# Optimization experiments

Measured on AMD Instinct MI355X. Metric: run time of the kernel, lower is better.

Reference implementation:

```python
import jax, jax.numpy as jnp
import numpy as np

B, T, H, M = 16, 1024, 512, 80
NHEADS, HDIM = 8, H // 8


def _p(key, shape, scale=0.05):
    return scale * jax.random.normal(key, shape, dtype=jnp.float32)


def setup_inputs() -> dict:
    key = jax.random.key(0)
    ks = jax.random.split(key, 20)
    return {
        "encoder_memory": jax.random.normal(ks[0], (B, T, H), dtype=jnp.float32),
        "target_mel": jax.random.normal(ks[1], (B, T, M), dtype=jnp.float32),
        # prenet Linear(mel_dim -> hidden_dim)
        "w_prenet": _p(ks[2], (H, M)), "b_prenet": _p(ks[3], (H,)),
        # MultiheadAttention packed in-proj (3H, H) and out-proj (H, H)
        "in_proj_w": _p(ks[4], (3 * H, H)), "in_proj_b": _p(ks[5], (3 * H,)),
        "out_proj_w": _p(ks[6], (H, H)), "out_proj_b": _p(ks[7], (H,)),
        # 2-layer LSTM (torch gate order i,f,g,o); h0=c0=0 each step so W_hh acts on zeros
        "w_ih0": _p(ks[8], (4 * H, 2 * H)), "w_hh0": _p(ks[9], (4 * H, H)),
        "b_ih0": _p(ks[10], (4 * H,)), "b_hh0": _p(ks[11], (4 * H,)),
        "w_ih1": _p(ks[12], (4 * H, H)), "w_hh1": _p(ks[13], (4 * H, H)),
        "b_ih1": _p(ks[14], (4 * H,)), "b_hh1": _p(ks[15], (4 * H,)),
        # mel projection Linear(hidden_dim -> mel_dim)
        "w_mel": _p(ks[16], (M, H)), "b_mel": _p(ks[17], (M,)),
    }


def _lstm_cell_zero_state(x, w_ih, w_hh, b_ih, b_hh):
    # single step from zero (h, c): the W_hh @ h0 term is exactly zero
    gates = x @ w_ih.T + (b_ih + b_hh)  # (B,T,4H)
    i, f, g, o = jnp.split(gates, 4, axis=-1)
    c = jax.nn.sigmoid(i) * jnp.tanh(g)  # f * c_prev == 0
    return jax.nn.sigmoid(o) * jnp.tanh(c)


def reference(encoder_memory, target_mel, w_prenet, b_prenet,
              in_proj_w, in_proj_b, out_proj_w, out_proj_b,
              w_ih0, w_hh0, b_ih0, b_hh0, w_ih1, w_hh1, b_ih1, b_hh1,
              w_mel, b_mel):
    # teacher forcing: prev_mel at step t is zeros (t=0) else target_mel[:, t-1]
    prev = jnp.concatenate(
        [jnp.zeros((B, 1, M), dtype=target_mel.dtype), target_mel[:, :-1]], axis=1)
    pre = jax.nn.relu(prev @ w_prenet.T + b_prenet)  # (B,T,H); dropout is identity (eval)

    # cross-attention: each step's length-1 query attends over all encoder frames,
    # which vectorizes to standard (no-mask) MHA with queries = pre
    wq, wk, wv = jnp.split(in_proj_w, 3, axis=0)
    bq, bk, bv = jnp.split(in_proj_b, 3, axis=0)
    q = (pre @ wq.T + bq).reshape(B, T, NHEADS, HDIM)
    k = (encoder_memory @ wk.T + bk).reshape(B, T, NHEADS, HDIM)
    v = (encoder_memory @ wv.T + bv).reshape(B, T, NHEADS, HDIM)
    scale = 1.0 / jnp.sqrt(jnp.float32(HDIM))
    scores = jnp.einsum('bqhd,bkhd->bhqk', q * scale, k)  # (B,8,T,T)
    attn = jax.nn.softmax(scores, axis=-1)
    ctx = jnp.einsum('bhqk,bkhd->bqhd', attn, v).reshape(B, T, H)
    attn_out = ctx @ out_proj_w.T + out_proj_b  # (B,T,H)

    dec_in = jnp.concatenate([pre, attn_out], axis=-1)  # (B,T,2H)
    h1 = _lstm_cell_zero_state(dec_in, w_ih0, w_hh0, b_ih0, b_hh0)
    h2 = _lstm_cell_zero_state(h1, w_ih1, w_hh1, b_ih1, b_hh1)
    return h2 @ w_mel.T + b_mel  # (B,T,M)
```

## Files before the change

### kernel.cpp

```cpp
#include <hip/hip_runtime.h>


typedef _Float16 f16;
typedef _Float16 f16x8 __attribute__((ext_vector_type(8)));
typedef _Float16 f16x4 __attribute__((ext_vector_type(4)));
typedef float f32x4 __attribute__((ext_vector_type(4)));

constexpr int B_ = 16, T_ = 1024, H_ = 512, M_ = 80;
constexpr int NH_ = 8, D_ = 64;
constexpr int N_ = B_ * T_;

#define MFMA16(a, b, c) __builtin_amdgcn_mfma_f32_16x16x32_f16(a, b, c, 0, 0, 0)

__device__ __forceinline__ void gload_lds16(const f16* g, f16* l) {
  __builtin_amdgcn_global_load_lds(
      (const __attribute__((address_space(1))) void*)g,
      (__attribute__((address_space(3))) void*)l, 16, 0, 0);
}

template <int EPI, bool CONCATA, bool NCHK>
__global__ __launch_bounds__(256) void mgemm(
    const f16* __restrict__ A, const f16* __restrict__ A2,
    const f16* __restrict__ Wt, const float* __restrict__ bias,
    const float* __restrict__ bias2, float scale, void* __restrict__ outp,
    int K, int N) {
  __shared__ f16 As[128 * 64];
  __shared__ f16 Bs[128 * 64];
  const int tid = threadIdx.x;
  const int lane = tid & 63, wid = tid >> 6;
  const int lq = lane & 15, lg = lane >> 4;
  const int wm = wid >> 1, wn = wid & 1;
  const int r0 = blockIdx.x * 128, c0 = blockIdx.y * 128;

  f32x4 acc[4][4] = {};

  for (int k0 = 0; k0 < K; k0 += 64) {
#pragma unroll
    for (int it = 0; it < 4; ++it) {
      const int off = it * 4096 + wid * 1024 + lane * 16;
      const int row = off >> 7;
      const int cb = (off >> 4) & 7;
      const int kc = k0 + ((cb ^ (row & 7)) << 3);
      const f16* src;
      if (CONCATA) {
        src = (kc < 512) ? (A + (size_t)(r0 + row) * 512 + kc)
                         : (A2 + (size_t)(r0 + row) * 512 + (kc - 512));
      } else {
        src = A + (size_t)(r0 + row) * K + kc;
      }
      gload_lds16(src, (f16*)((char*)As + off));
    }
#pragma unroll
    for (int it = 0; it < 4; ++it) {
      const int off = it * 4096 + wid * 1024 + lane * 16;
      const int row = off >> 7;
      const int cb = (off >> 4) & 7;
      int crow = c0 + row;
      if (NCHK) crow = crow < N ? crow : N - 1;
      gload_lds16(Wt + (size_t)crow * K + k0 + ((cb ^ (row & 7)) << 3),
                  (f16*)((char*)Bs + off));
    }
    __syncthreads();
#pragma unroll
    for (int kk = 0; kk < 2; ++kk) {
      f16x8 af[4], bf[4];
#pragma unroll
      for (int m = 0; m < 4; ++m) {
        const int row = wm * 64 + m * 16 + lq;
        af[m] = *(const f16x8*)((const char*)As + row * 128 +
                                (((kk * 4 + lg) ^ (row & 7)) << 4));
      }
#pragma unroll
      for (int n = 0; n < 4; ++n) {
        const int row = wn * 64 + n * 16 + lq;
        bf[n] = *(const f16x8*)((const char*)Bs + row * 128 +
                                (((kk * 4 + lg) ^ (row & 7)) << 4));
      }
#pragma unroll
      for (int m = 0; m < 4; ++m)
#pragma unroll
        for (int n = 0; n < 4; ++n) acc[m][n] = MFMA16(af[m], bf[n], acc[m][n]);
    }
    __syncthreads();
  }

#pragma unroll
  for (int m = 0; m < 4; ++m) {
    const int rbase = r0 + wm * 64 + m * 16 + lg * 4;
#pragma unroll
    for (int n = 0; n < 4; ++n) {
      const int col = c0 + wn * 64 + n * 16 + lq;
      if (NCHK && col >= N) continue;
      const float bsum = bias[col] + (bias2 ? bias2[col] : 0.f);
      const f32x4 a = acc[m][n];
      if (EPI == 3) {
        const int b = rbase >> 10, t = rbase & (T_ - 1);
        const int head = col >> 6, d = col & 63;
        f16x4 pk;
#pragma unroll
        for (int r = 0; r < 4; ++r) pk[r] = (f16)((a[r] + bsum) * scale);
        *(f16x4*)((f16*)outp + ((size_t)((b * NH_ + head) * D_ + d)) * T_ + t) =
            pk;
      } else {
#pragma unroll
        for (int r = 0; r < 4; ++r) {
          const int row = rbase + r;
          float v = (a[r] + bsum) * scale;
          if (EPI == 1) v = fmaxf(v, 0.f);
          if (EPI == 4)
            ((float*)outp)[(size_t)row * N + col] = v;
          else
            ((f16*)outp)[(size_t)row * N + col] = (f16)v;
        }
      }
    }
  }
}

template <bool CONCATA>
__global__ __launch_bounds__(512) void lstm_fused(
    const f16* __restrict__ A, const f16* __restrict__ A2,
    const f16* __restrict__ Wih, const float* __restrict__ bih,
    const float* __restrict__ bhh, f16* __restrict__ Hout_) {
  constexpr int K = CONCATA ? 1024 : 512;
  __shared__ f16 As[128 * 64];
  __shared__ f16 Bs[3][128 * 64];
  const int tid = threadIdx.x;
  const int lane = tid & 63, wid = tid >> 6;
  const int lq = lane & 15, lg = lane >> 4;
  const int wm = wid >> 1, wn = wid & 1;
  const int r0 = blockIdx.x * 128, c0 = blockIdx.y * 128;

  f32x4 acc[3][2][4] = {};

  for (int k0 = 0; k0 < K; k0 += 64) {
#pragma unroll
    for (int it = 0; it < 2; ++it) {
      const int off = it * 8192 + tid * 16;
      const int row = off >> 7;
      const int cb = (off >> 4) & 7;
      const int kc = k0 + ((cb ^ (row & 7)) << 3);
      const f16* src;
      if (CONCATA) {
        src = (kc < 512) ? (A + (size_t)(r0 + row) * 512 + kc)
                         : (A2 + (size_t)(r0 + row) * 512 + (kc - 512));
      } else {
        src = A + (size_t)(r0 + row) * K + kc;
      }
      gload_lds16(src, (f16*)((char*)As + off));
    }
#pragma unroll
    for (int g = 0; g < 3; ++g) {
      const int gbase = (g == 0) ? 0 : 512 * (g + 1);
#pragma unroll
      for (int it = 0; it < 2; ++it) {
        const int off = it * 8192 + tid * 16;
        const int row = off >> 7;
        const int cb = (off >> 4) & 7;
        gload_lds16(
            Wih + (size_t)(gbase + c0 + row) * K + k0 + ((cb ^ (row & 7)) << 3),
            (f16*)((char*)&Bs[g][0] + off));
      }
    }
    __syncthreads();
#pragma unroll
    for (int kk = 0; kk < 2; ++kk) {
      f16x8 af[2];
#pragma unroll
      for (int m = 0; m < 2; ++m) {
        const int row = wm * 32 + m * 16 + lq;
        af[m] = *(const f16x8*)((const char*)As + row * 128 +
                                (((kk * 4 + lg) ^ (row & 7)) << 4));
      }
#pragma unroll
      for (int g = 0; g < 3; ++g)
#pragma unroll
        for (int n = 0; n < 4; ++n) {
          const int row = wn * 64 + n * 16 + lq;
          const f16x8 bf = *(const f16x8*)((const char*)&Bs[g][0] + row * 128 +
                                           (((kk * 4 + lg) ^ (row & 7)) << 4));
#pragma unroll
          for (int m = 0; m < 2; ++m)
            acc[g][m][n] = MFMA16(af[m], bf, acc[g][m][n]);
        }
    }
    __syncthreads();
  }

#pragma unroll
  for (int n = 0; n < 4; ++n) {
    const int c = c0 + wn * 64 + n * 16 + lq;
    const float bi = bih[c] + bhh[c];
    const float bg = bih[1024 + c] + bhh[1024 + c];
    const float bo = bih[1536 + c] + bhh[1536 + c];
#pragma unroll
    for (int m = 0; m < 2; ++m) {
      const int rbase = r0 + wm * 32 + m * 16 + lg * 4;
#pragma unroll
      for (int r = 0; r < 4; ++r) {
        const float gi = acc[0][m][n][r] + bi;
        const float gg = acc[1][m][n][r] + bg;
        const float go = acc[2][m][n][r] + bo;
        const float si = 1.f / (1.f + __expf(-gi));
        const float so = 1.f / (1.f + __expf(-go));
        const float tg = 2.f / (1.f + __expf(-2.f * gg)) - 1.f;
        const float cc = si * tg;
        const float tc = 2.f / (1.f + __expf(-2.f * cc)) - 1.f;
        Hout_[(size_t)(rbase + r) * 512 + c] = (f16)(so * tc);
      }
    }
  }
}

__global__ __launch_bounds__(256) void attn_mfma3(
    const f16* __restrict__ q, const f16* __restrict__ k,
    const f16* __restrict__ vT, f16* __restrict__ ctx) {
  __shared__ f16 Ks[2][64 * 64];
  __shared__ f16 Vs[2][64 * 64];
  __shared__ f16 Ps[4][16 * 64];
  const int qt = blockIdx.x, head = blockIdx.y, b = blockIdx.z;
  const int tid = threadIdx.x, lane = tid & 63, wid = tid >> 6;
  const int lq = lane & 15, lg = lane >> 4;
  const int bh = b * NH_ + head;

  const f16* kbase = k + ((size_t)b * T_) * H_ + head * D_;
  const f16* vbase = vT + (size_t)bh * D_ * T_;

  auto stage = [&](int kt, int buf) {
#pragma unroll
    for (int it = 0; it < 2; ++it) {
      const int off = it * 4096 + tid * 16;
      const int row = off >> 7;
      const int sc = ((((off >> 4) & 7) ^ (row & 7)) << 3);
      gload_lds16(kbase + (size_t)(kt * 64 + row) * H_ + sc,
                  (f16*)((char*)&Ks[buf][0] + off));
      gload_lds16(vbase + (size_t)row * T_ + kt * 64 + sc,
                  (f16*)((char*)&Vs[buf][0] + off));
    }
  };

  const int q0 = qt * 128 + wid * 32;
  f16x8 qf[2][2];
#pragma unroll
  for (int s = 0; s < 2; ++s)
#pragma unroll
    for (int kk = 0; kk < 2; ++kk)
      qf[s][kk] = *(const f16x8*)(q + ((size_t)(b * T_) + q0 + s * 16 + lq) * H_ +
                                  head * D_ + kk * 32 + lg * 8);

  float m_run[2] = {-1e30f, -1e30f}, l_run[2] = {0.f, 0.f};
  f32x4 accO[2][4] = {};
  char* pw = (char*)&Ps[wid][0] + lq * 128;
  const int psw = (lq & 3) << 5;

  stage(0, 0);
  __syncthreads();

  for (int kt = 0; kt < T_ / 64; ++kt) {
    const int cur = kt & 1;
    if (kt < T_ / 64 - 1) stage(kt + 1, cur ^ 1);

    f16x8 kf[4][2];
#pragma unroll
    for (int n = 0; n < 4; ++n)
#pragma unroll
      for (int kk = 0; kk < 2; ++kk) {
        const int row = n * 16 + lq;
        kf[n][kk] = *(const f16x8*)((const char*)&Ks[cur][0] + row * 128 +
                                    (((kk * 4 + lg) ^ (row & 7)) << 4));
      }
    f32x4 ssw[2][4] = {};
    __builtin_amdgcn_s_setprio(1);
#pragma unroll
    for (int s = 0; s < 2; ++s)
#pragma unroll
      for (int n = 0; n < 4; ++n)
#pragma unroll
        for (int kk = 0; kk < 2; ++kk)
          ssw[s][n] = MFMA16(kf[n][kk], qf[s][kk], ssw[s][n]);
    __builtin_amdgcn_s_setprio(0);

    f16x8 vf[4][2];
#pragma unroll
    for (int n = 0; n < 4; ++n)
#pragma unroll
      for (int kk = 0; kk < 2; ++kk) {
        const int row = n * 16 + lq;
        vf[n][kk] = *(const f16x8*)((const char*)&Vs[cur][0] + row * 128 +
                                    (((kk * 4 + lg) ^ (row & 7)) << 4));
      }

#pragma unroll
    for (int s = 0; s < 2; ++s) {
      float mloc = -1e30f;
#pragma unroll
      for (int n = 0; n < 4; ++n)
#pragma unroll
        for (int r = 0; r < 4; ++r) mloc = fmaxf(mloc, ssw[s][n][r]);
      mloc = fmaxf(mloc, __shfl_xor(mloc, 16, 64));
      mloc = fmaxf(mloc, __shfl_xor(mloc, 32, 64));

      const bool noresc = __all(mloc - m_run[s] <= 8.f);
      if (!noresc) {
        const float nm = fmaxf(m_run[s], mloc);
        const float corr = __expf(m_run[s] - nm);
        m_run[s] = nm;
        l_run[s] *= corr;
#pragma unroll
        for (int n = 0; n < 4; ++n) {
          accO[s][n][0] *= corr; accO[s][n][1] *= corr;
          accO[s][n][2] *= corr; accO[s][n][3] *= corr;
        }
      }
      float sl = 0.f;
#pragma unroll
      for (int n = 0; n < 4; ++n) {
        f16x4 pk;
#pragma unroll
        for (int r = 0; r < 4; ++r) {
          const float p = __expf(ssw[s][n][r] - m_run[s]);
          sl += p;
          pk[r] = (f16)p;
        }
        *(f16x4*)(pw + ((n * 32 + lg * 8) ^ psw)) = pk;
      }
      sl += __shfl_xor(sl, 16, 64);
      sl += __shfl_xor(sl, 32, 64);
      l_run[s] += sl;

      f16x8 pb[2];
#pragma unroll
      for (int kk = 0; kk < 2; ++kk)
        pb[kk] = *(const f16x8*)(pw + ((((kk * 4 + lg) << 4)) ^ psw));
      __builtin_amdgcn_s_setprio(1);
#pragma unroll
      for (int n = 0; n < 4; ++n)
#pragma unroll
        for (int kk = 0; kk < 2; ++kk)
          accO[s][n] = MFMA16(vf[n][kk], pb[kk], accO[s][n]);
      __builtin_amdgcn_s_setprio(0);
    }
    __syncthreads();
  }

#pragma unroll
  for (int s = 0; s < 2; ++s) {
    const float inv = 1.f / l_run[s];
    const size_t rowoff = ((size_t)(b * T_) + q0 + s * 16 + lq) * H_ + head * D_;
#pragma unroll
    for (int n = 0; n < 4; ++n) {
      f16x4 o;
#pragma unroll
      for (int r = 0; r < 4; ++r) o[r] = (f16)(accO[s][n][r] * inv);
      *(f16x4*)(ctx + rowoff + n * 16 + lg * 4) = o;
    }
  }
}

constexpr int C0 = 2097152;
constexpr int C1 = C0 + 196608;
constexpr int C2 = C1 + 65536;
constexpr int C3 = C2 + 524288;
constexpr int C4 = C3 + 262144;
constexpr int C5 = C4 + 10240;
__global__ void conv_all(const float* __restrict__ enc, const float* __restrict__ inw,
                         const float* __restrict__ outw, const float* __restrict__ wih0,
                         const float* __restrict__ wih1, const float* __restrict__ wmel,
                         f16* denc, f16* dinw, f16* doutw, f16* dwih0,
                         f16* dwih1, f16* dwmel) {
  const int i = blockIdx.x * blockDim.x + threadIdx.x;
  const float* s;
  f16* d;
  int off;
  if (i < C0) { s = enc; d = denc; off = i; }
  else if (i < C1) { s = inw; d = dinw; off = i - C0; }
  else if (i < C2) { s = outw; d = doutw; off = i - C1; }
  else if (i < C3) { s = wih0; d = dwih0; off = i - C2; }
  else if (i < C4) { s = wih1; d = dwih1; off = i - C3; }
  else if (i < C5) { s = wmel; d = dwmel; off = i - C4; }
  else return;
  const float4 v = ((const float4*)s)[off];
  f16x4 o = {(f16)v.x, (f16)v.y, (f16)v.z, (f16)v.w};
  ((f16x4*)d)[off] = o;
}

__global__ void build_pm(const float* __restrict__ tmel, f16* __restrict__ pm) {
  const int i = blockIdx.x * blockDim.x + threadIdx.x;
  const int r = i >> 5, c4 = (i & 31) * 4;
  const int t = r & (T_ - 1);
  f16x4 o = {};
  if (t != 0 && c4 < M_) {
    const float4 v = *(const float4*)(tmel + (size_t)(r - 1) * M_ + c4);
    o = {(f16)v.x, (f16)v.y, (f16)v.z, (f16)v.w};
  }
  *(f16x4*)(pm + (size_t)r * 128 + c4) = o;
}

__global__ void build_wp(const float* __restrict__ w, f16* __restrict__ wp) {
  const int i = blockIdx.x * blockDim.x + threadIdx.x;
  const int r = i >> 5, c4 = (i & 31) * 4;
  f16x4 o = {};
  if (c4 < M_) {
    const float4 v = *(const float4*)(w + (size_t)r * M_ + c4);
    o = {(f16)v.x, (f16)v.y, (f16)v.z, (f16)v.w};
  }
  *(f16x4*)(wp + (size_t)r * 128 + c4) = o;
}

extern "C" void kernel_launch(void* const* d_in, const int* in_sizes, int n_in,
                              void* d_out, int out_size, void* d_ws,
                              size_t ws_size, hipStream_t stream) {
  const float* enc = (const float*)d_in[0];
  const float* tmel = (const float*)d_in[1];
  const float* w_pre = (const float*)d_in[2];
  const float* b_pre = (const float*)d_in[3];
  const float* inw = (const float*)d_in[4];
  const float* inb = (const float*)d_in[5];
  const float* outw = (const float*)d_in[6];
  const float* outb = (const float*)d_in[7];
  const float* wih0 = (const float*)d_in[8];
  const float* bih0 = (const float*)d_in[10];
  const float* bhh0 = (const float*)d_in[11];
  const float* wih1 = (const float*)d_in[12];
  const float* bih1 = (const float*)d_in[14];
  const float* bhh1 = (const float*)d_in[15];
  const float* wmel = (const float*)d_in[16];
  const float* bmel = (const float*)d_in[17];

  f16* wsh = (f16*)d_ws;
  const size_t SEG = (size_t)N_ * H_;
  f16* EncB = wsh;
  f16* h1 = wsh + SEG;
  f16* pre = wsh + 2 * SEG;
  f16* qb = wsh + 3 * SEG;
  f16* kbuf = wsh + 4 * SEG;
  f16* vTb = wsh + 5 * SEG;
  f16* ctx = wsh + 6 * SEG;
  f16* aout = EncB;
  f16* h2 = qb;
  f16* WP = wsh + 7 * SEG;
  f16* WIN = WP + 512 * 128;
  f16* WOUT = WIN + 1536 * 512;
  f16* WIH0 = WOUT + 512 * 512;
  f16* WIH1 = WIH0 + 2048 * 1024;
  f16* WMEL = WIH1 + 2048 * 512;
  f16* PM = WMEL + 80 * 512;

  const dim3 blk(256);
  conv_all<<<(C5 + 255) / 256, blk, 0, stream>>>(enc, inw, outw, wih0, wih1,
                                                 wmel, EncB, WIN, WOUT, WIH0,
                                                 WIH1, WMEL);
  build_pm<<<(N_ * 32) / 256, blk, 0, stream>>>(tmel, PM);
  build_wp<<<(512 * 32) / 256, blk, 0, stream>>>(w_pre, WP);

  const dim3 g512(N_ / 128, 4), g80(N_ / 128, 1);
  mgemm<1, false, false><<<g512, blk, 0, stream>>>(PM, nullptr, WP, b_pre,
                                                   nullptr, 1.f, pre, 128, 512);
  mgemm<0, false, false><<<g512, blk, 0, stream>>>(pre, nullptr, WIN, inb,
                                                   nullptr, 0.125f, qb, 512, 512);
  mgemm<0, false, false><<<g512, blk, 0, stream>>>(
      EncB, nullptr, WIN + 512 * 512, inb + 512, nullptr, 1.f, kbuf, 512, 512);
  mgemm<3, false, false><<<g512, blk, 0, stream>>>(
      EncB, nullptr, WIN + 1024 * 512, inb + 1024, nullptr, 1.f, vTb, 512, 512);
  attn_mfma3<<<dim3(T_ / 128, NH_, B_), blk, 0, stream>>>(qb, kbuf, vTb, ctx);
  mgemm<0, false, false><<<g512, blk, 0, stream>>>(ctx, nullptr, WOUT, outb,
                                                   nullptr, 1.f, aout, 512, 512);
  lstm_fused<true><<<dim3(N_ / 128, 4), dim3(512), 0, stream>>>(
      pre, aout, WIH0, bih0, bhh0, h1);
  lstm_fused<false><<<dim3(N_ / 128, 4), dim3(512), 0, stream>>>(
      h1, nullptr, WIH1, bih1, bhh1, h2);
  mgemm<4, false, true><<<g80, blk, 0, stream>>>(h2, nullptr, WMEL, bmel,
                                                 nullptr, 1.f, (float*)d_out,
                                                 512, 80);
}
```

Measured before the change: 308.5 us.

## Fuse K and V projections into one GEMM and retile LSTM to 256 threads

Replaces the separate K and V projection GEMMs with one kv_fused kernel that loads each encoder tile once and computes both outputs, writing V in transposed layout. The LSTM gate kernel moves from 512 threads with 2x4 MFMA tiles per wave to 256 threads with 4x4 tiles per wave and a two-blocks-per-CU launch bound. The aim is to halve reads of encoder memory and raise MFMA work per LDS fragment load. The larger accumulator arrays (48 and 32 f32x4 per thread) raise register pressure and may reduce occupancy.

```diff
diff --git a/kernel.cpp b/kernel.cpp
--- a/kernel.cpp
+++ b/kernel.cpp
@@ -118,7 +118,7 @@
 }
 
 template <bool CONCATA>
-__global__ __launch_bounds__(512) void lstm_fused(
+__global__ __launch_bounds__(256, 2) void lstm_fused(
     const f16* __restrict__ A, const f16* __restrict__ A2,
     const f16* __restrict__ Wih, const float* __restrict__ bih,
     const float* __restrict__ bhh, f16* __restrict__ Hout_) {
@@ -131,12 +131,12 @@
   const int wm = wid >> 1, wn = wid & 1;
   const int r0 = blockIdx.x * 128, c0 = blockIdx.y * 128;
 
-  f32x4 acc[3][2][4] = {};
+  f32x4 acc[3][4][4] = {};
 
   for (int k0 = 0; k0 < K; k0 += 64) {
 #pragma unroll
-    for (int it = 0; it < 2; ++it) {
-      const int off = it * 8192 + tid * 16;
+    for (int it = 0; it < 4; ++it) {
+      const int off = it * 4096 + tid * 16;
       const int row = off >> 7;
       const int cb = (off >> 4) & 7;
       const int kc = k0 + ((cb ^ (row & 7)) << 3);
@@ -153,8 +153,8 @@
     for (int g = 0; g < 3; ++g) {
       const int gbase = (g == 0) ? 0 : 512 * (g + 1);
 #pragma unroll
-      for (int it = 0; it < 2; ++it) {
-        const int off = it * 8192 + tid * 16;
+      for (int it = 0; it < 4; ++it) {
+        const int off = it * 4096 + tid * 16;
         const int row = off >> 7;
         const int cb = (off >> 4) & 7;
         gload_lds16(
@@ -165,10 +165,10 @@
     __syncthreads();
 #pragma unroll
     for (int kk = 0; kk < 2; ++kk) {
-      f16x8 af[2];
-#pragma unroll
-      for (int m = 0; m < 2; ++m) {
-        const int row = wm * 32 + m * 16 + lq;
+      f16x8 af[4];
+#pragma unroll
+      for (int m = 0; m < 4; ++m) {
+        const int row = wm * 64 + m * 16 + lq;
         af[m] = *(const f16x8*)((const char*)As + row * 128 +
                                 (((kk * 4 + lg) ^ (row & 7)) << 4));
       }
@@ -180,7 +180,7 @@
           const f16x8 bf = *(const f16x8*)((const char*)&Bs[g][0] + row * 128 +
                                            (((kk * 4 + lg) ^ (row & 7)) << 4));
 #pragma unroll
-          for (int m = 0; m < 2; ++m)
+          for (int m = 0; m < 4; ++m)
             acc[g][m][n] = MFMA16(af[m], bf, acc[g][m][n]);
         }
     }
@@ -194,8 +194,8 @@
     const float bg = bih[1024 + c] + bhh[1024 + c];
     const float bo = bih[1536 + c] + bhh[1536 + c];
 #pragma unroll
-    for (int m = 0; m < 2; ++m) {
-      const int rbase = r0 + wm * 32 + m * 16 + lg * 4;
+    for (int m = 0; m < 4; ++m) {
+      const int rbase = r0 + wm * 64 + m * 16 + lg * 4;
 #pragma unroll
       for (int r = 0; r < 4; ++r) {
         const float gi = acc[0][m][n][r] + bi;
@@ -208,6 +208,88 @@
         const float tc = 2.f / (1.f + __expf(-2.f * cc)) - 1.f;
         Hout_[(size_t)(rbase + r) * 512 + c] = (f16)(so * tc);
       }
+    }
+  }
+}
+
+__global__ __launch_bounds__(256, 2) void kv_fused(
+    const f16* __restrict__ A, const f16* __restrict__ Wt,
+    const float* __restrict__ bias, f16* __restrict__ kout,
+    f16* __restrict__ vout) {
+  constexpr int K = 512;
+  __shared__ f16 As[128 * 64];
+  __shared__ f16 Bs[2][128 * 64];
+  const int tid = threadIdx.x;
+  const int lane = tid & 63, wid = tid >> 6;
+  const int lq = lane & 15, lg = lane >> 4;
+  const int wm = wid >> 1, wn = wid & 1;
+  const int r0 = blockIdx.x * 128, c0 = blockIdx.y * 128;
+
+  f32x4 acc[2][4][4] = {};
+
+  for (int k0 = 0; k0 < K; k0 += 64) {
+#pragma unroll
+    for (int it = 0; it < 4; ++it) {
+      const int off = it * 4096 + tid * 16;
+      const int row = off >> 7;
+      const int cb = (off >> 4) & 7;
+      const int kc = k0 + ((cb ^ (row & 7)) << 3);
+      gload_lds16(A + (size_t)(r0 + row) * K + kc, (f16*)((char*)As + off));
+    }
+#pragma unroll
+    for (int g = 0; g < 2; ++g) {
+#pragma unroll
+      for (int it = 0; it < 4; ++it) {
+        const int off = it * 4096 + tid * 16;
+        const int row = off >> 7;
+        const int cb = (off >> 4) & 7;
+        gload_lds16(
+            Wt + (size_t)(g * 512 + c0 + row) * K + k0 + ((cb ^ (row & 7)) << 3),
+            (f16*)((char*)&Bs[g][0] + off));
+      }
+    }
+    __syncthreads();
+#pragma unroll
+    for (int kk = 0; kk < 2; ++kk) {
+      f16x8 af[4];
+#pragma unroll
+      for (int m = 0; m < 4; ++m) {
+        const int row = wm * 64 + m * 16 + lq;
+        af[m] = *(const f16x8*)((const char*)As + row * 128 +
+                                (((kk * 4 + lg) ^ (row & 7)) << 4));
+      }
+#pragma unroll
+      for (int g = 0; g < 2; ++g)
+#pragma unroll
+        for (int n = 0; n < 4; ++n) {
+          const int row = wn * 64 + n * 16 + lq;
+          const f16x8 bf = *(const f16x8*)((const char*)&Bs[g][0] + row * 128 +
+                                           (((kk * 4 + lg) ^ (row & 7)) << 4));
+#pragma unroll
+          for (int m = 0; m < 4; ++m)
+            acc[g][m][n] = MFMA16(af[m], bf, acc[g][m][n]);
+        }
+    }
+    __syncthreads();
+  }
+
+#pragma unroll
+  for (int m = 0; m < 4; ++m) {
+    const int rbase = r0 + wm * 64 + m * 16 + lg * 4;
+    const int b = rbase >> 10, t = rbase & (T_ - 1);
+#pragma unroll
+    for (int n = 0; n < 4; ++n) {
+      const int col = c0 + wn * 64 + n * 16 + lq;
+      const float bk = bias[col];
+#pragma unroll
+      for (int r = 0; r < 4; ++r)
+        kout[(size_t)(rbase + r) * 512 + col] = (f16)(acc[0][m][n][r] + bk);
+      const float bv = bias[512 + col];
+      const int head = col >> 6, d = col & 63;
+      f16x4 pk;
+#pragma unroll
+      for (int r = 0; r < 4; ++r) pk[r] = (f16)(acc[1][m][n][r] + bv);
+      *(f16x4*)(vout + ((size_t)((b * NH_ + head) * D_ + d)) * T_ + t) = pk;
     }
   }
 }
@@ -458,17 +540,13 @@
                                                    nullptr, 1.f, pre, 128, 512);
   mgemm<0, false, false><<<g512, blk, 0, stream>>>(pre, nullptr, WIN, inb,
                                                    nullptr, 0.125f, qb, 512, 512);
-  mgemm<0, false, false><<<g512, blk, 0, stream>>>(
-      EncB, nullptr, WIN + 512 * 512, inb + 512, nullptr, 1.f, kbuf, 512, 512);
-  mgemm<3, false, false><<<g512, blk, 0, stream>>>(
-      EncB, nullptr, WIN + 1024 * 512, inb + 1024, nullptr, 1.f, vTb, 512, 512);
+  kv_fused<<<g512, blk, 0, stream>>>(EncB, WIN + 512 * 512, inb + 512, kbuf,
+                                     vTb);
   attn_mfma3<<<dim3(T_ / 128, NH_, B_), blk, 0, stream>>>(qb, kbuf, vTb, ctx);
   mgemm<0, false, false><<<g512, blk, 0, stream>>>(ctx, nullptr, WOUT, outb,
                                                    nullptr, 1.f, aout, 512, 512);
-  lstm_fused<true><<<dim3(N_ / 128, 4), dim3(512), 0, stream>>>(
-      pre, aout, WIH0, bih0, bhh0, h1);
-  lstm_fused<false><<<dim3(N_ / 128, 4), dim3(512), 0, stream>>>(
-      h1, nullptr, WIH1, bih1, bhh1, h2);
+  lstm_fused<true><<<g512, blk, 0, stream>>>(pre, aout, WIH0, bih0, bhh0, h1);
+  lstm_fused<false><<<g512, blk, 0, stream>>>(h1, nullptr, WIH1, bih1, bhh1, h2);
   mgemm<4, false, true><<<g80, blk, 0, stream>>>(h2, nullptr, WMEL, bmel,
                                                  nullptr, 1.f, (float*)d_out,
                                                  512, 80);
```

New measurement: 285.7 us. 1.08x faster.
